# Performance work log

Hardware: AMD Instinct MI355X
Metric: run time of the kernel (lower is better)

## Reference

```python
import jax, jax.numpy as jnp
import numpy as np

B, N, D, H, C = 4, 512, 128, 128, 3


def setup_inputs() -> dict:
    key = jax.random.key(0)
    k1, k2, k3, k4, k5 = jax.random.split(key, 5)
    s1 = 1.0 / np.sqrt(2 * D)  # torch Linear default init scale (uniform bound); randn is fine for a numerics baseline
    s2 = 1.0 / np.sqrt(H)
    return {
        "h_dense": jax.random.normal(k1, (B, N, D), dtype=jnp.float32),
        "W1": jax.random.normal(k2, (H, 2 * D), dtype=jnp.float32) * s1,
        "b1": jax.random.normal(k3, (H,), dtype=jnp.float32) * s1,
        "W2": jax.random.normal(k4, (C, H), dtype=jnp.float32) * s2,
        "b2": jax.random.normal(k5, (C,), dtype=jnp.float32) * s2,
    }


def reference(h_dense, W1, b1, W2, b2):
    # Linear(concat(h_src, h_dst)) == h_src @ W1[:, :D].T + h_dst @ W1[:, D:].T + b1
    # which avoids materializing the (B, N, N, 2D) concat tensor (same math).
    d = h_dense.shape[-1]
    a = jnp.einsum("bnd,hd->bnh", h_dense, W1[:, :d])  # src projection (B, N, H)
    b = jnp.einsum("bnd,hd->bnh", h_dense, W1[:, d:])  # dst projection (B, N, H)
    pre = a[:, :, None, :] + b[:, None, :, :] + b1      # (B, N, N, H)
    act = jax.nn.silu(pre)
    logits = jnp.einsum("bijh,ch->bijc", act, W2) + b2  # (B, N, N, C)
    # symmetrize over the pair axes (dropout is identity in eval mode)
    return (logits + jnp.swapaxes(logits, 1, 2)) * 0.5
```

## Files before the change

kernel.cpp:

```cpp
#include <hip/hip_runtime.h>
#include <hip/hip_fp16.h>

#define B_ 4
#define N_ 512
#define D_ 128
#define H_ 128
#define C_ 3

#define NEG_LOG2E   (-1.4426950408889634f)
#define NEG_HALF_LN2 (-0.34657359027997264f)
#define ROWP 136

typedef _Float16 half8  __attribute__((ext_vector_type(8)));
typedef _Float16 half4v __attribute__((ext_vector_type(4)));

__device__ __forceinline__ float exp2_fast(float x) {
    return __builtin_amdgcn_exp2f(x);
}

__global__ __launch_bounds__(256) void proj_gemm(
    const float* __restrict__ hd, const float* __restrict__ W1,
    const float* __restrict__ b1, _Float16* __restrict__ At, _Float16* __restrict__ Bt)
{
    __shared__ float hsT[64][36];
    __shared__ float wt [64][68];
    const int m0      = blockIdx.x * 32;
    const int by      = blockIdx.y;
    const int halfSel = by >> 1;
    const int wrow0   = (by & 1) * 64;

    const int t  = threadIdx.x;
    const int r  = t >> 4, c4 = t & 15;
    const int tx = t & 15, ty = t >> 4;

    float acc[2][4] = {};

    for (int kc = 0; kc < 2; ++kc) {
        if (kc) __syncthreads();
        #pragma unroll
        for (int i = 0; i < 2; ++i) {
            const int m = r + 16 * i;
            float4 v = *(const float4*)&hd[(m0 + m) * D_ + kc * 64 + 4 * c4];
            hsT[4 * c4 + 0][m] = v.x; hsT[4 * c4 + 1][m] = v.y;
            hsT[4 * c4 + 2][m] = v.z; hsT[4 * c4 + 3][m] = v.w;
        }
        #pragma unroll
        for (int i = 0; i < 4; ++i) {
            const int o = r + 16 * i;
            float4 v = *(const float4*)&W1[(wrow0 + o) * (2 * D_) + halfSel * D_ + kc * 64 + 4 * c4];
            wt[4 * c4 + 0][o] = v.x; wt[4 * c4 + 1][o] = v.y;
            wt[4 * c4 + 2][o] = v.z; wt[4 * c4 + 3][o] = v.w;
        }
        __syncthreads();
        #pragma unroll 8
        for (int k = 0; k < 64; ++k) {
            float2 a  = *(const float2*)&hsT[k][2 * ty];
            float4 bv = *(const float4*)&wt [k][4 * tx];
            acc[0][0] = fmaf(a.x, bv.x, acc[0][0]); acc[0][1] = fmaf(a.x, bv.y, acc[0][1]);
            acc[0][2] = fmaf(a.x, bv.z, acc[0][2]); acc[0][3] = fmaf(a.x, bv.w, acc[0][3]);
            acc[1][0] = fmaf(a.y, bv.x, acc[1][0]); acc[1][1] = fmaf(a.y, bv.y, acc[1][1]);
            acc[1][2] = fmaf(a.y, bv.z, acc[1][2]); acc[1][3] = fmaf(a.y, bv.w, acc[1][3]);
        }
    }

    _Float16* dst = halfSel ? Bt : At;
    const int ocol = wrow0 + 4 * tx;
    float4 bias = make_float4(0.f, 0.f, 0.f, 0.f);
    if (!halfSel) bias = *(const float4*)&b1[ocol];
    #pragma unroll
    for (int i = 0; i < 2; ++i) {
        half4v o;
        o[0] = (_Float16)((acc[i][0] + bias.x) * NEG_LOG2E);
        o[1] = (_Float16)((acc[i][1] + bias.y) * NEG_LOG2E);
        o[2] = (_Float16)((acc[i][2] + bias.z) * NEG_LOG2E);
        o[3] = (_Float16)((acc[i][3] + bias.w) * NEG_LOG2E);
        *(half4v*)&dst[(m0 + 2 * ty + i) * H_ + ocol] = o;
    }
}

__global__ __launch_bounds__(256, 4) void pair_kernel(
    const _Float16* __restrict__ At, const _Float16* __restrict__ Bt,
    const float* __restrict__ W2, const float* __restrict__ b2,
    float* __restrict__ out)
{
    __shared__ __align__(16) _Float16 AI[16 * ROWP], AJ[16 * ROWP];
    __shared__ __align__(16) _Float16 BI[16 * ROWP], BJ[16 * ROWP];
    const int T = N_ / 16;
    int tp = blockIdx.x;
    const int b = blockIdx.y;
    int I = 0;
    while (tp >= T - I) { tp -= T - I; ++I; }
    const int J = I + tp;

    const int tid = threadIdx.x;
    {
        const int r = tid >> 4, c = (tid & 15) * 8;
        const half8* sAI = (const half8*)(At + (b * N_ + I * 16) * H_);
        const half8* sAJ = (const half8*)(At + (b * N_ + J * 16) * H_);
        const half8* sBI = (const half8*)(Bt + (b * N_ + I * 16) * H_);
        const half8* sBJ = (const half8*)(Bt + (b * N_ + J * 16) * H_);
        *(half8*)&AI[r * ROWP + c] = sAI[tid];
        *(half8*)&AJ[r * ROWP + c] = sAJ[tid];
        *(half8*)&BI[r * ROWP + c] = sBI[tid];
        *(half8*)&BJ[r * ROWP + c] = sBJ[tid];
    }
    __syncthreads();

    const int ti = tid >> 4, tj = tid & 15;
    float acc0a = 0.f, acc1a = 0.f, acc2a = 0.f;
    float acc0b = 0.f, acc1b = 0.f, acc2b = 0.f;

    #pragma unroll 4
    for (int h8 = 0; h8 < H_ / 8; ++h8) {
        const int hb = h8 * 8;
        half8 ai8 = *(const half8*)&AI[ti * ROWP + hb];
        half8 bj8 = *(const half8*)&BJ[tj * ROWP + hb];
        half8 aj8 = *(const half8*)&AJ[tj * ROWP + hb];
        half8 bi8 = *(const half8*)&BI[ti * ROWP + hb];
        half8 y1h = ai8 + bj8;
        half8 y2h = aj8 + bi8;
        float y1[8], y2[8], d1[8], d2[8], s[8];
        #pragma unroll
        for (int e = 0; e < 8; ++e) { y1[e] = (float)y1h[e]; y2[e] = (float)y2h[e]; }
        #pragma unroll
        for (int e = 0; e < 8; ++e) { d1[e] = 1.0f + exp2_fast(y1[e]); }
        #pragma unroll
        for (int e = 0; e < 8; ++e) { d2[e] = 1.0f + exp2_fast(y2[e]); }
        #pragma unroll
        for (int e = 0; e < 8; ++e) {
            const float rr = __builtin_amdgcn_rcpf(d1[e] * d2[e]);
            s[e] = fmaf(y2[e], d1[e], y1[e] * d2[e]) * rr;
        }
        float4 w0a = *(const float4*)&W2[hb],          w0b = *(const float4*)&W2[hb + 4];
        float4 w1a = *(const float4*)&W2[H_ + hb],     w1b = *(const float4*)&W2[H_ + hb + 4];
        float4 w2a = *(const float4*)&W2[2 * H_ + hb], w2b = *(const float4*)&W2[2 * H_ + hb + 4];
        const float w0[8] = {w0a.x, w0a.y, w0a.z, w0a.w, w0b.x, w0b.y, w0b.z, w0b.w};
        const float w1[8] = {w1a.x, w1a.y, w1a.z, w1a.w, w1b.x, w1b.y, w1b.z, w1b.w};
        const float w2[8] = {w2a.x, w2a.y, w2a.z, w2a.w, w2b.x, w2b.y, w2b.z, w2b.w};
        #pragma unroll
        for (int e = 0; e < 8; e += 2) {
            acc0a = fmaf(s[e],     w0[e],     acc0a);
            acc1a = fmaf(s[e],     w1[e],     acc1a);
            acc2a = fmaf(s[e],     w2[e],     acc2a);
            acc0b = fmaf(s[e + 1], w0[e + 1], acc0b);
            acc1b = fmaf(s[e + 1], w1[e + 1], acc1b);
            acc2b = fmaf(s[e + 1], w2[e + 1], acc2b);
        }
    }

    const float o0 = fmaf(NEG_HALF_LN2, acc0a + acc0b, b2[0]);
    const float o1 = fmaf(NEG_HALF_LN2, acc1a + acc1b, b2[1]);
    const float o2 = fmaf(NEG_HALF_LN2, acc2a + acc2b, b2[2]);
    const int i = I * 16 + ti, j = J * 16 + tj;
    float* p1 = out + ((size_t)(b * N_ + i) * N_ + j) * C_;
    float* p2 = out + ((size_t)(b * N_ + j) * N_ + i) * C_;
    p1[0] = o0; p1[1] = o1; p1[2] = o2;
    p2[0] = o0; p2[1] = o1; p2[2] = o2;
}

extern "C" void kernel_launch(void* const* d_in, const int* in_sizes, int n_in,
                              void* d_out, int out_size, void* d_ws, size_t ws_size,
                              hipStream_t stream) {
    const float* hd = (const float*)d_in[0];
    const float* W1 = (const float*)d_in[1];
    const float* b1 = (const float*)d_in[2];
    const float* W2 = (const float*)d_in[3];
    const float* b2 = (const float*)d_in[4];
    float* out = (float*)d_out;

    _Float16* At = (_Float16*)d_ws;
    _Float16* Bt = At + B_ * N_ * H_;

    proj_gemm<<<dim3((B_ * N_) / 32, 4), dim3(256), 0, stream>>>(hd, W1, b1, At, Bt);

    const int T = N_ / 16;
    pair_kernel<<<dim3(T * (T + 1) / 2, B_), dim3(256), 0, stream>>>(At, Bt, W2, b2, out);
}
```

Baseline: 43.23 us.

## Precompute per-row exp2 tiles so pair loop multiplies instead of exponentiating

The staging step now computes exp2 of each projected row once and stores it next to the raw values in shared memory. The pair loop then forms exp2(a+b) as a product of the two stored factors, which removes the two transcendentals per pair element. Most of the sigmoid arithmetic also moves into packed fp16, the H dimension is staged in two halves, and an XOR swizzle replaces the padded row layout to avoid bank conflicts. The risks are fp16 overflow or precision loss in the products d1*d2 and num, plus an extra barrier between the halves.

Result: faster. 39.25 us (-9.2%).

```diff
diff --git a/kernel.cpp b/kernel.cpp
--- a/kernel.cpp
+++ b/kernel.cpp
@@ -9,7 +9,6 @@
 
 #define NEG_LOG2E   (-1.4426950408889634f)
 #define NEG_HALF_LN2 (-0.34657359027997264f)
-#define ROWP 136
 
 typedef _Float16 half8  __attribute__((ext_vector_type(8)));
 typedef _Float16 half4v __attribute__((ext_vector_type(4)));
@@ -83,8 +82,7 @@
     const float* __restrict__ W2, const float* __restrict__ b2,
     float* __restrict__ out)
 {
-    __shared__ __align__(16) _Float16 AI[16 * ROWP], AJ[16 * ROWP];
-    __shared__ __align__(16) _Float16 BI[16 * ROWP], BJ[16 * ROWP];
+    __shared__ _Float16 tiles[8][16 * 64];
     const int T = N_ / 16;
     int tp = blockIdx.x;
     const int b = blockIdx.y;
@@ -93,58 +91,78 @@
     const int J = I + tp;
 
     const int tid = threadIdx.x;
-    {
-        const int r = tid >> 4, c = (tid & 15) * 8;
-        const half8* sAI = (const half8*)(At + (b * N_ + I * 16) * H_);
-        const half8* sAJ = (const half8*)(At + (b * N_ + J * 16) * H_);
-        const half8* sBI = (const half8*)(Bt + (b * N_ + I * 16) * H_);
-        const half8* sBJ = (const half8*)(Bt + (b * N_ + J * 16) * H_);
-        *(half8*)&AI[r * ROWP + c] = sAI[tid];
-        *(half8*)&AJ[r * ROWP + c] = sAJ[tid];
-        *(half8*)&BI[r * ROWP + c] = sBI[tid];
-        *(half8*)&BJ[r * ROWP + c] = sBJ[tid];
-    }
-    __syncthreads();
+    const int stile = tid >> 6;
+    const int srow  = (tid >> 2) & 15;
+    const int scc   = tid & 3;
+    const _Float16* gsrc = ((stile & 2) ? Bt : At)
+        + (size_t)(b * N_ + ((stile & 1) ? J : I) * 16 + srow) * H_;
+    _Float16* ybase = &tiles[stile][srow * 64];
+    _Float16* ebase = &tiles[stile + 4][srow * 64];
+    const int sxor = srow & 7;
 
     const int ti = tid >> 4, tj = tid & 15;
+    const int xI = ti & 7, xJ = tj & 7;
+
     float acc0a = 0.f, acc1a = 0.f, acc2a = 0.f;
     float acc0b = 0.f, acc1b = 0.f, acc2b = 0.f;
 
-    #pragma unroll 4
-    for (int h8 = 0; h8 < H_ / 8; ++h8) {
-        const int hb = h8 * 8;
-        half8 ai8 = *(const half8*)&AI[ti * ROWP + hb];
-        half8 bj8 = *(const half8*)&BJ[tj * ROWP + hb];
-        half8 aj8 = *(const half8*)&AJ[tj * ROWP + hb];
-        half8 bi8 = *(const half8*)&BI[ti * ROWP + hb];
-        half8 y1h = ai8 + bj8;
-        half8 y2h = aj8 + bi8;
-        float y1[8], y2[8], d1[8], d2[8], s[8];
+    for (int ph = 0; ph < 2; ++ph) {
+        if (ph) __syncthreads();
         #pragma unroll
-        for (int e = 0; e < 8; ++e) { y1[e] = (float)y1h[e]; y2[e] = (float)y2h[e]; }
-        #pragma unroll
-        for (int e = 0; e < 8; ++e) { d1[e] = 1.0f + exp2_fast(y1[e]); }
-        #pragma unroll
-        for (int e = 0; e < 8; ++e) { d2[e] = 1.0f + exp2_fast(y2[e]); }
-        #pragma unroll
-        for (int e = 0; e < 8; ++e) {
-            const float rr = __builtin_amdgcn_rcpf(d1[e] * d2[e]);
-            s[e] = fmaf(y2[e], d1[e], y1[e] * d2[e]) * rr;
+        for (int q = 0; q < 2; ++q) {
+            const int c = scc + 4 * q;
+            half8 yv = *(const half8*)&gsrc[ph * 64 + c * 8];
+            half8 ev;
+            #pragma unroll
+            for (int e = 0; e < 8; ++e)
+                ev[e] = (_Float16)exp2_fast((float)yv[e]);
+            const int cs = (c ^ sxor) * 8;
+            *(half8*)&ybase[cs] = yv;
+            *(half8*)&ebase[cs] = ev;
         }
-        float4 w0a = *(const float4*)&W2[hb],          w0b = *(const float4*)&W2[hb + 4];
-        float4 w1a = *(const float4*)&W2[H_ + hb],     w1b = *(const float4*)&W2[H_ + hb + 4];
-        float4 w2a = *(const float4*)&W2[2 * H_ + hb], w2b = *(const float4*)&W2[2 * H_ + hb + 4];
-        const float w0[8] = {w0a.x, w0a.y, w0a.z, w0a.w, w0b.x, w0b.y, w0b.z, w0b.w};
-        const float w1[8] = {w1a.x, w1a.y, w1a.z, w1a.w, w1b.x, w1b.y, w1b.z, w1b.w};
-        const float w2[8] = {w2a.x, w2a.y, w2a.z, w2a.w, w2b.x, w2b.y, w2b.z, w2b.w};
-        #pragma unroll
-        for (int e = 0; e < 8; e += 2) {
-            acc0a = fmaf(s[e],     w0[e],     acc0a);
-            acc1a = fmaf(s[e],     w1[e],     acc1a);
-            acc2a = fmaf(s[e],     w2[e],     acc2a);
-            acc0b = fmaf(s[e + 1], w0[e + 1], acc0b);
-            acc1b = fmaf(s[e + 1], w1[e + 1], acc1b);
-            acc2b = fmaf(s[e + 1], w2[e + 1], acc2b);
+        __syncthreads();
+
+        #pragma unroll 2
+        for (int c = 0; c < 8; ++c) {
+            const int oI = ti * 64 + ((c ^ xI) * 8);
+            const int oJ = tj * 64 + ((c ^ xJ) * 8);
+            half8 yAI = *(const half8*)&tiles[0][oI];
+            half8 yAJ = *(const half8*)&tiles[1][oJ];
+            half8 yBI = *(const half8*)&tiles[2][oI];
+            half8 yBJ = *(const half8*)&tiles[3][oJ];
+            half8 eAI = *(const half8*)&tiles[4][oI];
+            half8 eAJ = *(const half8*)&tiles[5][oJ];
+            half8 eBI = *(const half8*)&tiles[6][oI];
+            half8 eBJ = *(const half8*)&tiles[7][oJ];
+
+            half8 y1 = yAI + yBJ;
+            half8 y2 = yAJ + yBI;
+            half8 e1 = eAI * eBJ;
+            half8 e2 = eAJ * eBI;
+            half8 d1 = e1 + (_Float16)1.0f;
+            half8 d2 = e2 + (_Float16)1.0f;
+            half8 pp = d1 * d2;
+            half8 num = y1 * d2 + y2 * d1;
+
+            const int hb = ph * 64 + c * 8;
+            float4 w0a = *(const float4*)&W2[hb],          w0b = *(const float4*)&W2[hb + 4];
+            float4 w1a = *(const float4*)&W2[H_ + hb],     w1b = *(const float4*)&W2[H_ + hb + 4];
+            float4 w2a = *(const float4*)&W2[2 * H_ + hb], w2b = *(const float4*)&W2[2 * H_ + hb + 4];
+            const float w0[8] = {w0a.x, w0a.y, w0a.z, w0a.w, w0b.x, w0b.y, w0b.z, w0b.w};
+            const float w1[8] = {w1a.x, w1a.y, w1a.z, w1a.w, w1b.x, w1b.y, w1b.z, w1b.w};
+            const float w2[8] = {w2a.x, w2a.y, w2a.z, w2a.w, w2b.x, w2b.y, w2b.z, w2b.w};
+
+            #pragma unroll
+            for (int e = 0; e < 8; e += 2) {
+                const float sa = (float)num[e]     * __builtin_amdgcn_rcpf((float)pp[e]);
+                const float sb = (float)num[e + 1] * __builtin_amdgcn_rcpf((float)pp[e + 1]);
+                acc0a = fmaf(sa, w0[e],     acc0a);
+                acc1a = fmaf(sa, w1[e],     acc1a);
+                acc2a = fmaf(sa, w2[e],     acc2a);
+                acc0b = fmaf(sb, w0[e + 1], acc0b);
+                acc1b = fmaf(sb, w1[e + 1], acc1b);
+                acc2b = fmaf(sb, w2[e + 1], acc2b);
+            }
         }
     }
 
```
